# Kernel optimization log

Hardware: AMD Instinct MI355X
Metric: run time of the kernel (lower is better)

## Reference

```python
import math
import jax, jax.numpy as jnp
import numpy as np

D_MODEL = 1024
N_HEADS = 16
D_K = D_MODEL // N_HEADS
LQ, LK, B = 2048, 2048, 2


def setup_inputs() -> dict:
    key = jax.random.key(0)
    ks = jax.random.split(key, 12)
    q = jax.random.normal(ks[0], (LQ, B, D_MODEL), dtype=jnp.float32)
    k = jax.random.normal(ks[1], (LK, B, D_MODEL), dtype=jnp.float32)
    v = jax.random.normal(ks[2], (LK, B, D_MODEL), dtype=jnp.float32)
    # causal mask: scores with mask==0 are filled with -1e9
    mask = jnp.tril(jnp.ones((LQ, LK), dtype=jnp.int32))
    s = 0.02
    w_q = jax.random.normal(ks[3], (D_MODEL, D_MODEL), jnp.float32) * s
    b_q = jnp.zeros((D_MODEL,), jnp.float32)
    w_k = jax.random.normal(ks[4], (D_MODEL, D_MODEL), jnp.float32) * s
    b_k = jnp.zeros((D_MODEL,), jnp.float32)
    w_v = jax.random.normal(ks[5], (D_MODEL, D_MODEL), jnp.float32) * s
    b_v = jnp.zeros((D_MODEL,), jnp.float32)
    w_o = jax.random.normal(ks[6], (D_MODEL, D_MODEL), jnp.float32) * s
    b_o = jnp.zeros((D_MODEL,), jnp.float32)
    return {"query": q, "key": k, "value": v, "mask": mask,
            "w_q": w_q, "b_q": b_q, "w_k": w_k, "b_k": b_k,
            "w_v": w_v, "b_v": b_v, "w_o": w_o, "b_o": b_o}


def reference(query, key, value, mask, w_q, b_q, w_k, b_k, w_v, b_v, w_o, b_o):
    # dropout layers are identity (eval mode)
    Lq, Bsz, D = query.shape
    Lk = key.shape[0]
    scale = math.sqrt(D_K)
    # seq-first linear projections, then [L,B,D] -> [B,H,L,dk]
    def proj(x, w, b, L):
        y = x @ w.T + b
        return y.reshape(L, Bsz, N_HEADS, D_K).transpose(1, 2, 0, 3)
    Q = proj(query, w_q, b_q, Lq)   # [B,H,Lq,dk]
    K = proj(key, w_k, b_k, Lk)     # [B,H,Lk,dk]
    V = proj(value, w_v, b_v, Lk)   # [B,H,Lk,dk]
    scores = jnp.einsum('bhqd,bhkd->bhqk', Q, K) / scale
    m = mask[None, None, :, :]  # 2D mask broadcast path of original
    scores = jnp.where(m == 0, jnp.float32(-1e9), scores)
    attn = jax.nn.softmax(scores, axis=-1)  # [B,H,Lq,Lk]
    out = jnp.einsum('bhqk,bhkd->bhqd', attn, V)  # [B,H,Lq,dk]
    # replicate torch: transpose(0,1) -> [H,B,Lq,dk], flat view to [Lq,B,D]
    out = jnp.transpose(out, (1, 0, 2, 3)).reshape(Lq, Bsz, D)
    output = out @ w_o.T + b_o
    return output, attn
```

## Files before the change

### kernel.cpp

```cpp
#include <hip/hip_runtime.h>
#include <cstdint>

#define DM    1024
#define NH    16
#define DKH   64
#define SEQ   2048
#define BSZ   2
#define MROWS 4096

typedef __attribute__((ext_vector_type(8))) short bf16x8;
typedef __attribute__((ext_vector_type(4))) float f32x4;

__device__ __forceinline__ f32x4 mfma16(bf16x8 a, bf16x8 b, f32x4 c){
  return __builtin_amdgcn_mfma_f32_16x16x32_bf16(a, b, c, 0, 0, 0);
}

__device__ __forceinline__ ushort f2bf(float f){
  unsigned u = __float_as_uint(f);
  return (ushort)((u + 0x7FFFu + ((u >> 16) & 1u)) >> 16);
}

__device__ __forceinline__ void gload16(const ushort* g, ushort* l){
  __builtin_amdgcn_global_load_lds(
      (const __attribute__((address_space(1))) void*)g,
      (__attribute__((address_space(3))) void*)l, 16, 0, 0);
}

__device__ __forceinline__ void ntstore4(float* p, f32x4 v){
  __builtin_nontemporal_store(v, (f32x4*)p);
}

__global__ void cast_all(const float* __restrict__ q, const float* __restrict__ k,
                         const float* __restrict__ v, const float* __restrict__ wq,
                         const float* __restrict__ wk, const float* __restrict__ wv,
                         const float* __restrict__ wo,
                         ushort* __restrict__ qb, ushort* __restrict__ kb,
                         ushort* __restrict__ vb, ushort* __restrict__ wqb,
                         ushort* __restrict__ wkb, ushort* __restrict__ wvb,
                         ushort* __restrict__ wob)
{
  const int NB = (MROWS*DM)/4;
  const int NW = (DM*DM)/4;
  int stride = gridDim.x*blockDim.x;
  for (int i = blockIdx.x*blockDim.x + threadIdx.x; i < 3*NB; i += stride){
    int sel = i >> 20, j = i & (NB-1);
    const float4 x = ((const float4*)(sel==0?q:sel==1?k:v))[j];
    ushort4 o; o.x=f2bf(x.x); o.y=f2bf(x.y); o.z=f2bf(x.z); o.w=f2bf(x.w);
    ((ushort4*)(sel==0?qb:sel==1?kb:vb))[j] = o;
  }
  for (int i = blockIdx.x*blockDim.x + threadIdx.x; i < 4*NW; i += stride){
    int sel = i >> 18, j = i & (NW-1);
    const float4 x = ((const float4*)(sel==0?wq:sel==1?wk:sel==2?wv:wo))[j];
    ushort4 o; o.x=f2bf(x.x); o.y=f2bf(x.y); o.z=f2bf(x.z); o.w=f2bf(x.w);
    ((ushort4*)(sel==0?wqb:sel==1?wkb:sel==2?wvb:wob))[j] = o;
  }
}

__device__ __forceinline__ void gemm_body128(const ushort* __restrict__ A,
                                             const ushort* __restrict__ W,
                                             const float* __restrict__ bias,
                                             ushort* __restrict__ outp)
{
  __shared__ ushort As[128*32];
  __shared__ ushort Bs[128*32];
  const int tid = threadIdx.x, w = tid>>6, l = tid&63;
  const int wr = w>>1, wc = w&1, lr = l&15, lg = l>>4;
  const int bm = blockIdx.x, bn = blockIdx.y;
  const ushort* Ab = A + (size_t)bm*128*DM;
  const ushort* Wb = W + (size_t)bn*128*DM;
  f32x4 z4 = {0.f,0.f,0.f,0.f};
  f32x4 acc[4][4];
  #pragma unroll
  for (int i=0;i<4;i++){ acc[i][0]=z4; acc[i][1]=z4; acc[i][2]=z4; acc[i][3]=z4; }

  for (int k0 = 0; k0 < DM; k0 += 32){
    __syncthreads();
    #pragma unroll
    for (int i=0;i<2;i++){
      int idx = w*2+i;
      int row = idx*16 + (l>>2);
      int cg  = (l&3)*8;
      gload16(&Ab[(size_t)row*DM + k0 + cg], &As[idx*512]);
      gload16(&Wb[(size_t)row*DM + k0 + cg], &Bs[idx*512]);
    }
    __syncthreads();
    bf16x8 af[4], bw[4];
    #pragma unroll
    for (int t=0;t<4;t++) af[t] = *(const bf16x8*)&As[(wr*64 + t*16 + lr)*32 + lg*8];
    #pragma unroll
    for (int t=0;t<4;t++) bw[t] = *(const bf16x8*)&Bs[(wc*64 + t*16 + lr)*32 + lg*8];
    #pragma unroll
    for (int tm=0;tm<4;tm++)
      #pragma unroll
      for (int tn=0;tn<4;tn++)
        acc[tm][tn] = mfma16(af[tm], bw[tn], acc[tm][tn]);
  }
  #pragma unroll
  for (int tn=0;tn<4;tn++){
    int col = bn*128 + wc*64 + tn*16 + lr;
    float bv = bias[col];
    #pragma unroll
    for (int tm=0;tm<4;tm++){
      #pragma unroll
      for (int r=0;r<4;r++){
        int row = bm*128 + wr*64 + tm*16 + lg*4 + r;
        outp[(size_t)row*DM + col] = f2bf(acc[tm][tn][r] + bv);
      }
    }
  }
}

__global__ __launch_bounds__(256) void gemm_qkv(
    const ushort* __restrict__ A0, const ushort* __restrict__ A1, const ushort* __restrict__ A2,
    const ushort* __restrict__ W0, const ushort* __restrict__ W1, const ushort* __restrict__ W2,
    const float* __restrict__ b0, const float* __restrict__ b1, const float* __restrict__ b2,
    ushort* __restrict__ O0, ushort* __restrict__ O1, ushort* __restrict__ O2)
{
  int z = blockIdx.z;
  const ushort* A = (z==0)?A0:((z==1)?A1:A2);
  const ushort* W = (z==0)?W0:((z==1)?W1:W2);
  const float*  b = (z==0)?b0:((z==1)?b1:b2);
  ushort*       O = (z==0)?O0:((z==1)?O1:O2);
  gemm_body128(A, W, b, O);
}

__global__ __launch_bounds__(256) void gemm_fin64(const ushort* __restrict__ A,
                                                  const ushort* __restrict__ W,
                                                  const float* __restrict__ bias,
                                                  float* __restrict__ O)
{
  __shared__ ushort As[64*32];
  __shared__ ushort Bs[128*32];
  const int tid = threadIdx.x, w = tid>>6, l = tid&63;
  const int wr = w>>1, wc = w&1, lr = l&15, lg = l>>4;
  const int bm = blockIdx.x, bn = blockIdx.y;
  const ushort* Ab = A + (size_t)bm*64*DM;
  const ushort* Wb = W + (size_t)bn*128*DM;
  f32x4 z4 = {0.f,0.f,0.f,0.f};
  f32x4 acc[2][4];
  #pragma unroll
  for (int i=0;i<2;i++){ acc[i][0]=z4; acc[i][1]=z4; acc[i][2]=z4; acc[i][3]=z4; }

  for (int k0 = 0; k0 < DM; k0 += 32){
    __syncthreads();
    {
      int row = w*16 + (l>>2);
      int cg  = (l&3)*8;
      gload16(&Ab[(size_t)row*DM + k0 + cg], &As[w*512]);
    }
    #pragma unroll
    for (int i=0;i<2;i++){
      int idx = w*2+i;
      int row = idx*16 + (l>>2);
      int cg  = (l&3)*8;
      gload16(&Wb[(size_t)row*DM + k0 + cg], &Bs[idx*512]);
    }
    __syncthreads();
    bf16x8 af[2], bw[4];
    #pragma unroll
    for (int t=0;t<2;t++) af[t] = *(const bf16x8*)&As[(wr*32 + t*16 + lr)*32 + lg*8];
    #pragma unroll
    for (int t=0;t<4;t++) bw[t] = *(const bf16x8*)&Bs[(wc*64 + t*16 + lr)*32 + lg*8];
    #pragma unroll
    for (int tm=0;tm<2;tm++)
      #pragma unroll
      for (int tn=0;tn<4;tn++)
        acc[tm][tn] = mfma16(af[tm], bw[tn], acc[tm][tn]);
  }
  #pragma unroll
  for (int tn=0;tn<4;tn++){
    int col = bn*128 + wc*64 + tn*16 + lr;
    float bv = bias[col];
    #pragma unroll
    for (int tm=0;tm<2;tm++){
      #pragma unroll
      for (int r=0;r<4;r++){
        int row = bm*64 + wr*32 + tm*16 + lg*4 + r;
        O[(size_t)row*DM + col] = acc[tm][tn][r] + bv;
      }
    }
  }
}

__global__ __launch_bounds__(256) void transpose_v(const ushort* __restrict__ Vp,
                                                   ushort* __restrict__ Vt)
{
  __shared__ ushort Ts[64*72];
  const int lt = blockIdx.x;
  const int h  = blockIdx.y;
  const int b  = blockIdx.z;
  const int tid = threadIdx.x;
  const int sr = tid>>3, sc = (tid&7)*8;
  uint4 v0 = *(const uint4*)&Vp[((size_t)(lt*64+sr)*BSZ + b)*DM + h*DKH + sc];
  uint4 v1 = *(const uint4*)&Vp[((size_t)(lt*64+sr+32)*BSZ + b)*DM + h*DKH + sc];
  const ushort* p0 = (const ushort*)&v0;
  const ushort* p1 = (const ushort*)&v1;
  #pragma unroll
  for (int j=0;j<8;j++){
    Ts[(sc+j)*72 + sr]    = p0[j];
    Ts[(sc+j)*72 + sr+32] = p1[j];
  }
  __syncthreads();
  const size_t ob = (size_t)((b*NH+h)*DKH);
  *(uint4*)&Vt[(ob + sr)*SEQ + lt*64 + sc]    = *(const uint4*)&Ts[sr*72 + sc];
  *(uint4*)&Vt[(ob + sr+32)*SEQ + lt*64 + sc] = *(const uint4*)&Ts[(sr+32)*72 + sc];
}

__global__ __launch_bounds__(256, 5) void attn_fused(const ushort* __restrict__ Qp,
                                                     const ushort* __restrict__ Kp,
                                                     const ushort* __restrict__ Vt,
                                                     float* __restrict__ attn,
                                                     ushort* __restrict__ ctx)
{
  __shared__ ushort Ks[64*72];
  __shared__ ushort Vs[64*72];
  __shared__ ushort Ps[4][16*72];
  const int bid0 = blockIdx.x;
  const int xcd = bid0 & 7, slot = bid0 >> 3;
  const int grp = xcd + 8*(slot & 3);
  const int ds  = slot >> 2;
  const int qt  = (ds & 1) ? (ds >> 1) : (31 - (ds >> 1));
  const int h = grp & 15, b = grp >> 4;
  const int q0 = qt*64;
  const int rounds = qt + 1;
  const int tid = threadIdx.x, w = tid>>6, l = tid&63;
  const int lr = l&15, lg = l>>4;
  ushort* Pw = &Ps[w][0];
  const size_t attnBase = (size_t)(b*NH+h)*SEQ*SEQ;
  const int qrow = q0 + w*16;
  const int sr = tid>>3, sc = (tid&7)*8;
  const ushort* Kg = Kp + (size_t)b*DM + h*DKH;
  const ushort* Vg = Vt + (size_t)((b*NH+h)*DKH)*SEQ;

  bf16x8 aq0 = *(const bf16x8*)&Qp[((size_t)(qrow+lr)*BSZ + b)*DM + h*DKH + lg*8];
  bf16x8 aq1 = *(const bf16x8*)&Qp[((size_t)(qrow+lr)*BSZ + b)*DM + h*DKH + 32 + lg*8];

  float rs[4] = {0.f,0.f,0.f,0.f};
  uint4 ka0 = *(const uint4*)&Kg[(size_t)(sr)*BSZ*DM + sc];
  uint4 ka1 = *(const uint4*)&Kg[(size_t)(sr+32)*BSZ*DM + sc];
  for (int r = 0; r < rounds; r++){
    __syncthreads();
    *(uint4*)&Ks[sr*72+sc]      = ka0;
    *(uint4*)&Ks[(sr+32)*72+sc] = ka1;
    if (r+1 < rounds){
      ka0 = *(const uint4*)&Kg[(size_t)((r+1)*64+sr)*BSZ*DM + sc];
      ka1 = *(const uint4*)&Kg[(size_t)((r+1)*64+sr+32)*BSZ*DM + sc];
    }
    __syncthreads();
    #pragma unroll
    for (int nt=0; nt<4; nt++){
      f32x4 s4 = {0.f,0.f,0.f,0.f};
      bf16x8 bk0 = *(const bf16x8*)&Ks[(nt*16+lr)*72 + lg*8];
      bf16x8 bk1 = *(const bf16x8*)&Ks[(nt*16+lr)*72 + 32 + lg*8];
      s4 = mfma16(aq0, bk0, s4);
      s4 = mfma16(aq1, bk1, s4);
      int kc = r*64 + nt*16 + lr;
      #pragma unroll
      for (int r4=0;r4<4;r4++){
        int qr = qrow + lg*4 + r4;
        float e = exp2f(s4[r4]*0.18033688011112042f);
        rs[r4] += (kc <= qr) ? e : 0.f;
      }
    }
  }
  float rinv[4];
  #pragma unroll
  for (int r4=0;r4<4;r4++){
    float vs = rs[r4];
    vs += __shfl_xor(vs, 1, 16);
    vs += __shfl_xor(vs, 2, 16);
    vs += __shfl_xor(vs, 4, 16);
    vs += __shfl_xor(vs, 8, 16);
    rinv[r4] = 1.0f / vs;
  }

  f32x4 z4 = {0.f,0.f,0.f,0.f};
  f32x4 oacc[4] = {z4,z4,z4,z4};
  uint4 kb0 = *(const uint4*)&Kg[(size_t)(sr)*BSZ*DM + sc];
  uint4 kb1 = *(const uint4*)&Kg[(size_t)(sr+32)*BSZ*DM + sc];
  uint4 vb0 = *(const uint4*)&Vg[(size_t)(sr)*SEQ + sc];
  uint4 vb1 = *(const uint4*)&Vg[(size_t)(sr+32)*SEQ + sc];
  __syncthreads();
  for (int r = 0; r < rounds; r++){
    __builtin_amdgcn_s_barrier();
    *(uint4*)&Ks[sr*72+sc]      = kb0;
    *(uint4*)&Ks[(sr+32)*72+sc] = kb1;
    *(uint4*)&Vs[sr*72+sc]      = vb0;
    *(uint4*)&Vs[(sr+32)*72+sc] = vb1;
    if (r+1 < rounds){
      kb0 = *(const uint4*)&Kg[(size_t)((r+1)*64+sr)*BSZ*DM + sc];
      kb1 = *(const uint4*)&Kg[(size_t)((r+1)*64+sr+32)*BSZ*DM + sc];
      vb0 = *(const uint4*)&Vg[(size_t)(sr)*SEQ + (r+1)*64 + sc];
      vb1 = *(const uint4*)&Vg[(size_t)(sr+32)*SEQ + (r+1)*64 + sc];
    }
    asm volatile("s_waitcnt lgkmcnt(0)" ::: "memory");
    __builtin_amdgcn_sched_barrier(0);
    __builtin_amdgcn_s_barrier();
    const int k0 = r*64;
    #pragma unroll
    for (int nt=0; nt<4; nt++){
      f32x4 s4 = {0.f,0.f,0.f,0.f};
      bf16x8 bk0 = *(const bf16x8*)&Ks[(nt*16+lr)*72 + lg*8];
      bf16x8 bk1 = *(const bf16x8*)&Ks[(nt*16+lr)*72 + 32 + lg*8];
      s4 = mfma16(aq0, bk0, s4);
      s4 = mfma16(aq1, bk1, s4);
      int kc = k0 + nt*16 + lr;
      #pragma unroll
      for (int r4=0;r4<4;r4++){
        int qg = qrow + lg*4 + r4;
        float p = (kc <= qg) ? exp2f(s4[r4]*0.18033688011112042f)*rinv[r4] : 0.f;
        Pw[(lg*4+r4)*72 + nt*16 + lr] = f2bf(p);
      }
    }
    #pragma unroll
    for (int pass=0; pass<4; pass++){
      int row16 = pass*4 + lg;
      ushort4 pv = *(const ushort4*)&Pw[row16*72 + lr*4];
      f32x4 o;
      o.x = __uint_as_float(((unsigned)pv.x) << 16);
      o.y = __uint_as_float(((unsigned)pv.y) << 16);
      o.z = __uint_as_float(((unsigned)pv.z) << 16);
      o.w = __uint_as_float(((unsigned)pv.w) << 16);
      ntstore4(&attn[attnBase + (size_t)(qrow + row16)*SEQ + k0 + lr*4], o);
    }
    bf16x8 pa0 = *(const bf16x8*)&Pw[lr*72 + lg*8];
    bf16x8 pa1 = *(const bf16x8*)&Pw[lr*72 + 32 + lg*8];
    #pragma unroll
    for (int nt=0; nt<4; nt++){
      bf16x8 vv0 = *(const bf16x8*)&Vs[(nt*16+lr)*72 + lg*8];
      bf16x8 vv1 = *(const bf16x8*)&Vs[(nt*16+lr)*72 + 32 + lg*8];
      oacc[nt] = mfma16(pa0, vv0, oacc[nt]);
      oacc[nt] = mfma16(pa1, vv1, oacc[nt]);
    }
  }
  #pragma unroll
  for (int nt=0;nt<4;nt++){
    #pragma unroll
    for (int r4=0;r4<4;r4++){
      int qg = qrow + lg*4 + r4;
      ctx[((size_t)(h*BSZ+b)*SEQ + qg)*DKH + nt*16 + lr] = f2bf(oacc[nt][r4]);
    }
  }
  int z0 = rounds*64;
  if (z0 < SEQ){
    f32x4 zz = {0.f,0.f,0.f,0.f};
    for (int r16=0; r16<16; r16++){
      float* rowp = attn + attnBase + (size_t)(qrow + r16)*SEQ;
      for (int c = z0 + l*4; c < SEQ; c += 256)
        ntstore4(&rowp[c], zz);
    }
  }
}

extern "C" void kernel_launch(void* const* d_in, const int* in_sizes, int n_in,
                              void* d_out, int out_size, void* d_ws, size_t ws_size,
                              hipStream_t stream)
{
  (void)in_sizes; (void)n_in; (void)out_size; (void)ws_size;
  const float* q  = (const float*)d_in[0];
  const float* k  = (const float*)d_in[1];
  const float* v  = (const float*)d_in[2];
  const float* wq = (const float*)d_in[4];
  const float* bq = (const float*)d_in[5];
  const float* wk = (const float*)d_in[6];
  const float* bk = (const float*)d_in[7];
  const float* wv = (const float*)d_in[8];
  const float* bv = (const float*)d_in[9];
  const float* wo = (const float*)d_in[10];
  const float* bo = (const float*)d_in[11];

  char* ws = (char*)d_ws;
  const size_t SZ_BIG = (size_t)MROWS*DM*2;
  const size_t SZ_W   = (size_t)DM*DM*2;
  ushort* Qb  = (ushort*)(ws);
  ushort* Kb  = (ushort*)(ws + SZ_BIG);
  ushort* Vb  = (ushort*)(ws + 2*SZ_BIG);
  ushort* Wqb = (ushort*)(ws + 3*SZ_BIG);
  ushort* Wkb = (ushort*)(ws + 3*SZ_BIG + SZ_W);
  ushort* Wvb = (ushort*)(ws + 3*SZ_BIG + 2*SZ_W);
  ushort* Wob = (ushort*)(ws + 3*SZ_BIG + 3*SZ_W);
  ushort* Qp  = (ushort*)(ws + 3*SZ_BIG + 4*SZ_W);
  ushort* Kp  = (ushort*)(ws + 4*SZ_BIG + 4*SZ_W);
  ushort* Vp  = (ushort*)(ws + 5*SZ_BIG + 4*SZ_W);
  ushort* Ctx = (ushort*)(ws + 6*SZ_BIG + 4*SZ_W);
  ushort* Vt  = Qb;

  float* out  = (float*)d_out;
  float* attn = out + (size_t)SEQ*BSZ*DM;

  cast_all<<<2048, 256, 0, stream>>>(q,k,v,wq,wk,wv,wo, Qb,Kb,Vb,Wqb,Wkb,Wvb,Wob);
  dim3 gq(32, 8, 3);
  gemm_qkv<<<gq, 256, 0, stream>>>(Qb,Kb,Vb, Wqb,Wkb,Wvb, bq,bk,bv, Qp,Kp,Vp);
  dim3 gt(32, NH, BSZ);
  transpose_v<<<gt, 256, 0, stream>>>(Vp, Vt);
  attn_fused<<<1024, 256, 0, stream>>>(Qp, Kp, Vt, attn, Ctx);
  dim3 gf(64, 8, 1);
  gemm_fin64<<<gf, 256, 0, stream>>>(Ctx, Wob, bo, out);
}
```

Measured before the change: 218.1 us.

## Split softmax row-sum pass into separate kernel with 128-row query tiles

The fused attention kernel's first pass (computing softmax denominators) moves into its own kernel. Each block now handles 128 query rows, with 32 rows per wave, so every K tile loaded into shared memory is reused across twice as many rows. The reciprocal sums are stored to a global workspace buffer, and the P·V kernel reads them back. This halves the K traffic for the sum pass, but adds one kernel launch and a small global round-trip, and the 512-block grid may balance causal work less evenly.

```diff
diff --git a/kernel.cpp b/kernel.cpp
--- a/kernel.cpp
+++ b/kernel.cpp
@@ -206,11 +206,82 @@
   *(uint4*)&Vt[(ob + sr+32)*SEQ + lt*64 + sc] = *(const uint4*)&Ts[(sr+32)*72 + sc];
 }
 
-__global__ __launch_bounds__(256, 5) void attn_fused(const ushort* __restrict__ Qp,
-                                                     const ushort* __restrict__ Kp,
-                                                     const ushort* __restrict__ Vt,
-                                                     float* __restrict__ attn,
-                                                     ushort* __restrict__ ctx)
+__global__ __launch_bounds__(256, 5) void attn_lsum(const ushort* __restrict__ Qp,
+                                                    const ushort* __restrict__ Kp,
+                                                    float* __restrict__ rinvG)
+{
+  __shared__ ushort Ks[64*72];
+  const int bid0 = blockIdx.x;
+  const int xcd = bid0 & 7, slot = bid0 >> 3;
+  const int grp = xcd + 8*(slot & 3);
+  const int qg  = slot >> 2;
+  const int h = grp & 15, b = grp >> 4;
+  const int tid = threadIdx.x, w = tid>>6, l = tid&63;
+  const int lr = l&15, lg = l>>4;
+  const int rounds = (qg+1)*2;
+  const int sr = tid>>3, sc = (tid&7)*8;
+  const ushort* Kg = Kp + (size_t)b*DM + h*DKH;
+  const int qrow0 = qg*128 + w*32;
+
+  bf16x8 aq0[2], aq1[2];
+  #pragma unroll
+  for (int s=0;s<2;s++){
+    const ushort* qp = &Qp[((size_t)(qrow0+s*16+lr)*BSZ + b)*DM + h*DKH];
+    aq0[s] = *(const bf16x8*)&qp[lg*8];
+    aq1[s] = *(const bf16x8*)&qp[32 + lg*8];
+  }
+
+  float rs[2][4] = {{0.f,0.f,0.f,0.f},{0.f,0.f,0.f,0.f}};
+  uint4 ka0 = *(const uint4*)&Kg[(size_t)(sr)*BSZ*DM + sc];
+  uint4 ka1 = *(const uint4*)&Kg[(size_t)(sr+32)*BSZ*DM + sc];
+  for (int r = 0; r < rounds; r++){
+    __syncthreads();
+    *(uint4*)&Ks[sr*72+sc]      = ka0;
+    *(uint4*)&Ks[(sr+32)*72+sc] = ka1;
+    if (r+1 < rounds){
+      ka0 = *(const uint4*)&Kg[(size_t)((r+1)*64+sr)*BSZ*DM + sc];
+      ka1 = *(const uint4*)&Kg[(size_t)((r+1)*64+sr+32)*BSZ*DM + sc];
+    }
+    __syncthreads();
+    #pragma unroll
+    for (int nt=0; nt<4; nt++){
+      bf16x8 bk0 = *(const bf16x8*)&Ks[(nt*16+lr)*72 + lg*8];
+      bf16x8 bk1 = *(const bf16x8*)&Ks[(nt*16+lr)*72 + 32 + lg*8];
+      int kc = r*64 + nt*16 + lr;
+      #pragma unroll
+      for (int s=0;s<2;s++){
+        f32x4 s4 = {0.f,0.f,0.f,0.f};
+        s4 = mfma16(aq0[s], bk0, s4);
+        s4 = mfma16(aq1[s], bk1, s4);
+        #pragma unroll
+        for (int r4=0;r4<4;r4++){
+          int qr = qrow0 + s*16 + lg*4 + r4;
+          float e = exp2f(s4[r4]*0.18033688011112042f);
+          rs[s][r4] += (kc <= qr) ? e : 0.f;
+        }
+      }
+    }
+  }
+  #pragma unroll
+  for (int s=0;s<2;s++)
+    #pragma unroll
+    for (int r4=0;r4<4;r4++){
+      float vs = rs[s][r4];
+      vs += __shfl_xor(vs, 1, 16);
+      vs += __shfl_xor(vs, 2, 16);
+      vs += __shfl_xor(vs, 4, 16);
+      vs += __shfl_xor(vs, 8, 16);
+      if (lr == 0)
+        rinvG[(size_t)(b*NH+h)*SEQ + qrow0 + s*16 + lg*4 + r4] = 1.0f / vs;
+    }
+}
+
+__global__ __launch_bounds__(256, 5) void attn_pv(const ushort* __restrict__ Qp,
+                                                  const ushort* __restrict__ Kp,
+                                                  const ushort* __restrict__ Vt,
+                                                  const float* __restrict__ rinvG,
+                                                  float* __restrict__ attn,
+                                                  ushort* __restrict__ ctx)
 {
   __shared__ ushort Ks[64*72];
   __shared__ ushort Vs[64*72];
@@ -235,44 +306,10 @@
   bf16x8 aq0 = *(const bf16x8*)&Qp[((size_t)(qrow+lr)*BSZ + b)*DM + h*DKH + lg*8];
   bf16x8 aq1 = *(const bf16x8*)&Qp[((size_t)(qrow+lr)*BSZ + b)*DM + h*DKH + 32 + lg*8];
 
-  float rs[4] = {0.f,0.f,0.f,0.f};
-  uint4 ka0 = *(const uint4*)&Kg[(size_t)(sr)*BSZ*DM + sc];
-  uint4 ka1 = *(const uint4*)&Kg[(size_t)(sr+32)*BSZ*DM + sc];
-  for (int r = 0; r < rounds; r++){
-    __syncthreads();
-    *(uint4*)&Ks[sr*72+sc]      = ka0;
-    *(uint4*)&Ks[(sr+32)*72+sc] = ka1;
-    if (r+1 < rounds){
-      ka0 = *(const uint4*)&Kg[(size_t)((r+1)*64+sr)*BSZ*DM + sc];
-      ka1 = *(const uint4*)&Kg[(size_t)((r+1)*64+sr+32)*BSZ*DM + sc];
-    }
-    __syncthreads();
-    #pragma unroll
-    for (int nt=0; nt<4; nt++){
-      f32x4 s4 = {0.f,0.f,0.f,0.f};
-      bf16x8 bk0 = *(const bf16x8*)&Ks[(nt*16+lr)*72 + lg*8];
-      bf16x8 bk1 = *(const bf16x8*)&Ks[(nt*16+lr)*72 + 32 + lg*8];
-      s4 = mfma16(aq0, bk0, s4);
-      s4 = mfma16(aq1, bk1, s4);
-      int kc = r*64 + nt*16 + lr;
-      #pragma unroll
-      for (int r4=0;r4<4;r4++){
-        int qr = qrow + lg*4 + r4;
-        float e = exp2f(s4[r4]*0.18033688011112042f);
-        rs[r4] += (kc <= qr) ? e : 0.f;
-      }
-    }
-  }
   float rinv[4];
   #pragma unroll
-  for (int r4=0;r4<4;r4++){
-    float vs = rs[r4];
-    vs += __shfl_xor(vs, 1, 16);
-    vs += __shfl_xor(vs, 2, 16);
-    vs += __shfl_xor(vs, 4, 16);
-    vs += __shfl_xor(vs, 8, 16);
-    rinv[r4] = 1.0f / vs;
-  }
+  for (int r4=0;r4<4;r4++)
+    rinv[r4] = rinvG[(size_t)(b*NH+h)*SEQ + qrow + lg*4 + r4];
 
   f32x4 z4 = {0.f,0.f,0.f,0.f};
   f32x4 oacc[4] = {z4,z4,z4,z4};
@@ -280,7 +317,6 @@
   uint4 kb1 = *(const uint4*)&Kg[(size_t)(sr+32)*BSZ*DM + sc];
   uint4 vb0 = *(const uint4*)&Vg[(size_t)(sr)*SEQ + sc];
   uint4 vb1 = *(const uint4*)&Vg[(size_t)(sr+32)*SEQ + sc];
-  __syncthreads();
   for (int r = 0; r < rounds; r++){
     __builtin_amdgcn_s_barrier();
     *(uint4*)&Ks[sr*72+sc]      = kb0;
@@ -383,6 +419,7 @@
   ushort* Kp  = (ushort*)(ws + 4*SZ_BIG + 4*SZ_W);
   ushort* Vp  = (ushort*)(ws + 5*SZ_BIG + 4*SZ_W);
   ushort* Ctx = (ushort*)(ws + 6*SZ_BIG + 4*SZ_W);
+  float*  Ls  = (float*)(ws + 7*SZ_BIG + 4*SZ_W);
   ushort* Vt  = Qb;
 
   float* out  = (float*)d_out;
@@ -393,7 +430,8 @@
   gemm_qkv<<<gq, 256, 0, stream>>>(Qb,Kb,Vb, Wqb,Wkb,Wvb, bq,bk,bv, Qp,Kp,Vp);
   dim3 gt(32, NH, BSZ);
   transpose_v<<<gt, 256, 0, stream>>>(Vp, Vt);
-  attn_fused<<<1024, 256, 0, stream>>>(Qp, Kp, Vt, attn, Ctx);
+  attn_lsum<<<512, 256, 0, stream>>>(Qp, Kp, Ls);
+  attn_pv<<<1024, 256, 0, stream>>>(Qp, Kp, Vt, Ls, attn, Ctx);
   dim3 gf(64, 8, 1);
   gemm_fin64<<<gf, 256, 0, stream>>>(Ctx, Wob, bo, out);
 }
```

Measured after the change: 258.9 us. +18.8%, slower.
